# Kernel tuning notes

Hardware: AMD Instinct MI355X
Metric: run time of the kernel (lower is better)

Reference implementation:

```python
import jax, jax.numpy as jnp
import numpy as np

NMS_THRESH = 0.3  # default nms_thresh in DetNet.predict


def setup_inputs() -> dict:
    key = jax.random.key(0)
    k1, k2, k3, k4 = jax.random.split(key, 4)
    W, N = 8, 1024
    det = jax.random.uniform(k1, (W, N, 5), dtype=jnp.float32)          # (conf, cx, cy, w, h) in [0,1)
    offsets = jax.random.uniform(k2, (W, 5), dtype=jnp.float32) * 0.5   # window offset vector (0, left, top, 0, 0)-like
    scales = jax.random.uniform(k3, (W, 5), dtype=jnp.float32) * 0.5 + 0.25  # window scale vector
    b = jax.random.uniform(k4, (W, 4), dtype=jnp.float32)
    # (valid_left, valid_right, valid_top, valid_bottom) with left<right, top<bottom
    bounds = jnp.stack([0.3 * b[:, 0], 0.7 + 0.3 * b[:, 1],
                        0.3 * b[:, 2], 0.7 + 0.3 * b[:, 3]], axis=-1)
    return {"det": det, "offsets": offsets, "scales": scales, "bounds": bounds}


def _pairwise_iou(boxes):
    # boxes: [M,4] in (x1,y1,x2,y2)
    x1, y1, x2, y2 = boxes[:, 0], boxes[:, 1], boxes[:, 2], boxes[:, 3]
    area = jnp.clip(x2 - x1, 0.0) * jnp.clip(y2 - y1, 0.0)              # [M]
    iw = jnp.clip(jnp.minimum(x2[:, None], x2[None, :]) - jnp.maximum(x1[:, None], x1[None, :]), 0.0)
    ih = jnp.clip(jnp.minimum(y2[:, None], y2[None, :]) - jnp.maximum(y1[:, None], y1[None, :]), 0.0)
    inter = iw * ih                                                     # [M,M]
    union = area[:, None] + area[None, :] - inter
    return inter / jnp.maximum(union, 1e-9)


def reference(det, offsets, scales, bounds):
    W, N, _ = det.shape
    M = W * N
    cx, cy = det[..., 1], det[..., 2]                                    # [W,N]
    left, right = bounds[:, 0:1], bounds[:, 1:2]
    top, bottom = bounds[:, 2:3], bounds[:, 3:4]
    valid = (cx < right) & (cx > left) & (cy < bottom) & (cy > top)      # [W,N] border mask
    # torch.addcmul(offset, d, scale) = offset + d * scale
    d = (offsets[:, None, :] + det * scales[:, None, :]).reshape(M, 5)
    valid = valid.reshape(M)
    scores = jnp.where(valid, d[:, 0], -1.0)                             # invalid boxes never kept
    order = jnp.argsort(-scores)                                         # descending confidence
    d_s = d[order]                                                       # [M,5]
    s_s = scores[order]
    # point_form: (cx,cy,w,h) -> (x1,y1,x2,y2)
    cxy, wh = d_s[:, 1:3], d_s[:, 3:5]
    boxes = jnp.concatenate([cxy - wh * 0.5, cxy + wh * 0.5], axis=-1)
    iou = jax.lax.stop_gradient(_pairwise_iou(boxes))                    # [M,M], suppression is non-diff
    s_c = jax.lax.stop_gradient(s_s)
    idx = jnp.arange(M)

    def body(i, keep):
        # suppressed if any kept higher-score box overlaps > thresh
        sup = jnp.any(keep & (idx < i) & (iou[:, i] > NMS_THRESH))
        return keep.at[i].set(jnp.logical_and(~sup, s_c[i] > 0.0))

    keep = jax.lax.fori_loop(0, M, body, jnp.ones((M,), dtype=bool))
    return d_s * keep[:, None].astype(d_s.dtype)                         # [M,5], suppressed rows zeroed
```

## Files before the change

kernel.cpp:

```cpp
#include <hip/hip_runtime.h>
#include <cstdint>


#define M_TOT 8192
#define NMS_T 0.3f

#define WS_BOX   65536
#define WS_D     196608
#define WS_VCNT  360448
#define WS_ZROW  393216
#define WS_MASK  524288

typedef unsigned long long u64t;

__device__ __forceinline__ uint32_t desc_key(float sv) {
    uint32_t u = __float_as_uint(sv);
    uint32_t m = (u & 0x80000000u) ? ~u : (u | 0x80000000u);
    return ~m;
}

__device__ __forceinline__ u64t rdl64(u64t v, int sl) {
    unsigned lo = (unsigned)__builtin_amdgcn_readlane((int)(unsigned)v, sl);
    unsigned hi = (unsigned)__builtin_amdgcn_readlane((int)(unsigned)(v >> 32), sl);
    return ((u64t)hi << 32) | lo;
}

__device__ __forceinline__ int scatter_one(
    int i, int rank, u64t key,
    const float* __restrict__ det, const float* __restrict__ offsets,
    const float* __restrict__ scales,
    float4* __restrict__ boxes_srt, float* __restrict__ d_srt)
{
    uint32_t dkey = (uint32_t)(key >> 16);
    if (dkey >= 0x7FFFFFFFu) return 0;
    int g = i >> 10;
    float d0 = __fadd_rn(offsets[g*5+0], __fmul_rn(det[i*5+0], scales[g*5+0]));
    float d1 = __fadd_rn(offsets[g*5+1], __fmul_rn(det[i*5+1], scales[g*5+1]));
    float d2 = __fadd_rn(offsets[g*5+2], __fmul_rn(det[i*5+2], scales[g*5+2]));
    float d3 = __fadd_rn(offsets[g*5+3], __fmul_rn(det[i*5+3], scales[g*5+3]));
    float d4 = __fadd_rn(offsets[g*5+4], __fmul_rn(det[i*5+4], scales[g*5+4]));
    d_srt[rank*5+0] = d0; d_srt[rank*5+1] = d1; d_srt[rank*5+2] = d2;
    d_srt[rank*5+3] = d3; d_srt[rank*5+4] = d4;
    float hw = __fmul_rn(d3, 0.5f), hh = __fmul_rn(d4, 0.5f);
    boxes_srt[rank] = make_float4(__fsub_rn(d1, hw), __fsub_rn(d2, hh),
                                  __fadd_rn(d1, hw), __fadd_rn(d2, hh));
    return 1;
}

__global__ __launch_bounds__(256) void k2_rank(
    const float* __restrict__ det, const float* __restrict__ offsets,
    const float* __restrict__ scales, const float* __restrict__ bounds,
    float4* __restrict__ boxes_srt, float* __restrict__ d_srt,
    unsigned int* __restrict__ vcnt, u64t* __restrict__ zrow,
    float* __restrict__ out)
{
    __shared__ u64t skey[M_TOT];
    __shared__ float soff[40], sscl[40], sbnd[32];
    __shared__ int sTop;
    int t = threadIdx.x;
    int lane = t & 63;
    if (t == 0) sTop = 0;
    if (t < 40) { soff[t] = offsets[t]; sscl[t] = scales[t]; }
    if (t < 32) { sbnd[t] = bounds[t]; }
    if (blockIdx.x == 0 && t < 128) zrow[t] = 0ull;
    __syncthreads();

    #pragma unroll 4
    for (int s = 0; s < 32; ++s) {
        int u = s * 256 + t;
        int g = u >> 10;
        float raw_s = det[u * 5 + 0];
        float cx    = det[u * 5 + 1];
        float cy    = det[u * 5 + 2];
        float score = __fadd_rn(soff[g * 5 + 0], __fmul_rn(raw_s, sscl[g * 5 + 0]));
        bool valid = (cx < sbnd[g*4+1]) && (cx > sbnd[g*4+0]) &&
                     (cy < sbnd[g*4+3]) && (cy > sbnd[g*4+2]);
        float sv = valid ? score : -1.0f;
        uint32_t dk = desc_key(sv);
        bool push = dk < 0x7FFFFFFFu;
        u64t key = ((u64t)dk << 16) | (unsigned)u;
        u64t bal = __ballot(push);
        if (bal) {
            int lw = 0;
            if (lane == 0) lw = atomicAdd(&sTop, __popcll(bal));
            int wbase = __builtin_amdgcn_readfirstlane(lw);
            if (push) {
                int off = __popcll(bal & ((1ull << lane) - 1ull));
                skey[wbase + off] = key;
            }
        }
    }
    __syncthreads();
    int V = sTop;
    int Vpad = (V + 15) & ~15;
    if (t < Vpad - V) skey[V + t] = ~0ull;
    {
        int zb = blockIdx.x * 160;
        for (int z = zb + t; z < zb + 160; z += 256) out[z] = 0.0f;
    }
    __syncthreads();
    if (t == 0) *vcnt = (unsigned)V;

    int grp = t >> 3;
    int jq  = t & 7;
    int i = blockIdx.x * 32 + grp;
    int g = i >> 10;
    float raw_s = det[i * 5 + 0];
    float cx    = det[i * 5 + 1];
    float cy    = det[i * 5 + 2];
    float score = __fadd_rn(soff[g * 5 + 0], __fmul_rn(raw_s, sscl[g * 5 + 0]));
    bool valid = (cx < sbnd[g*4+1]) && (cx > sbnd[g*4+0]) &&
                 (cy < sbnd[g*4+3]) && (cy > sbnd[g*4+2]);
    float sv = valid ? score : -1.0f;
    uint32_t dk = desc_key(sv);
    u64t ki = ((u64t)dk << 16) | (unsigned)i;
    const ulonglong2* skey2 = (const ulonglong2*)skey;
    int c = 0;
    int nit = Vpad >> 4;
    #pragma unroll 4
    for (int it = 0; it < nit; ++it) {
        ulonglong2 kj = skey2[it * 8 + jq];
        c += (kj.x < ki) + (kj.y < ki);
    }
    c += __shfl_xor(c, 1);
    c += __shfl_xor(c, 2);
    c += __shfl_xor(c, 4);
    if (jq == 0)
        scatter_one(i, c, ki, det, offsets, scales, boxes_srt, d_srt);
}

__global__ __launch_bounds__(256) void k_mask(
    const float4* __restrict__ boxes_srt,
    const unsigned int* __restrict__ vcnt,
    u64t* __restrict__ mask)
{
    __shared__ float4 sb[16 * 65];
    __shared__ float  sa[16 * 65];
    int V = (int)*vcnt;
    int bx = blockIdx.x, by = blockIdx.y;
    if (bx * 32 >= V) return;
    if (by * 1024 >= V) return;
    if (by * 16 + 15 < (bx * 32) >> 6) return;
    int nc = (V + 63) >> 6;
    int tid = threadIdx.x;
    int cbase = by * 1024;
    for (int u = tid; u < 1024; u += 256) {
        float4 b = boxes_srt[cbase + u];
        int c = u >> 6, jj = u & 63;
        sb[c * 65 + jj] = b;
        sa[c * 65 + jj] = __fmul_rn(fmaxf(__fsub_rn(b.z, b.x), 0.0f),
                                    fmaxf(__fsub_rn(b.w, b.y), 0.0f));
    }
    __syncthreads();
    int r = bx * 32 + (tid >> 3);
    if (r >= V) return;
    float4 bi = boxes_srt[r];
    float ai = __fmul_rn(fmaxf(__fsub_rn(bi.z, bi.x), 0.0f),
                         fmaxf(__fsub_rn(bi.w, bi.y), 0.0f));
    int rw = r >> 6;
    #pragma unroll
    for (int k = 0; k < 2; ++k) {
        int wl = (tid & 7) + k * 8;
        int w = by * 16 + wl;
        if (w < rw || w >= nc) continue;
        u64t bits = 0;
        #pragma unroll 4
        for (int jj = 0; jj < 64; ++jj) {
            float4 bj = sb[wl * 65 + jj];
            float aj = sa[wl * 65 + jj];
            float iw = fmaxf(__fsub_rn(fminf(bi.z, bj.z), fmaxf(bi.x, bj.x)), 0.0f);
            float ih = fmaxf(__fsub_rn(fminf(bi.w, bj.w), fmaxf(bi.y, bj.y)), 0.0f);
            float inter = __fmul_rn(iw, ih);
            float uni   = __fsub_rn(__fadd_rn(ai, aj), inter);
            float iou   = __fdiv_rn(inter, fmaxf(uni, 1e-9f));
            int j = w * 64 + jj;
            if (j > r && iou > NMS_T) bits |= 1ull << jj;
        }
        mask[(size_t)r * 128 + w] = bits;
    }
}

struct WSlot { ulonglong2 dl, dh, n1l, n1h, n2l, n2h; };

__device__ __forceinline__ void fill_words(
    const u64t* __restrict__ mask, int lane, int T, WSlot& w)
{
    int rl = min(T * 128 + lane,      M_TOT - 1);
    int rh = min(T * 128 + 64 + lane, M_TOT - 1);
    const ulonglong2* mrl = (const ulonglong2*)(mask + (size_t)rl * 128);
    const ulonglong2* mrh = (const ulonglong2*)(mask + (size_t)rh * 128);
    int p0 = min(T,     63);
    int p1 = min(T + 1, 63);
    int p2 = min(T + 2, 63);
    w.dl  = mrl[p0]; w.dh  = mrh[p0];
    w.n1l = mrl[p1]; w.n1h = mrh[p1];
    w.n2l = mrl[p2]; w.n2h = mrh[p2];
}

__device__ __forceinline__ void res_step(
    const u64t* __restrict__ mask,
    u64t* sdead, u64t* ck, volatile int* res_prog, volatile int* h_prog,
    int lane, int nc, int T,
    u64t& cA_lo, u64t& cA_hi, u64t& cB_lo, u64t& cB_hi, WSlot& w)
{
    if (T >= 3) {
        int need = T - 2;
        while (true) {
            int hp = (lane < 7) ? h_prog[lane] : 0x7FFFFFFF;
            if (__ballot(hp < need) == 0ull) break;
        }
    }
    u64t dlo = ((volatile u64t*)sdead)[2 * T];
    u64t dhi = ((volatile u64t*)sdead)[2 * T + 1];
    u64t live_lo = ~(dlo | cA_lo);
    u64t live_hi = ~(dhi | cA_hi);
    u64t km_lo = 0, km_hi = 0, c1l = 0, c1h = 0, c2l = 0, c2h = 0;
    while (live_lo | live_hi) {
        if (live_lo) {
            int bs = __builtin_amdgcn_readfirstlane(__builtin_ctzll(live_lo));
            u64t rml = rdl64(w.dl.x, bs), rmh = rdl64(w.dl.y, bs);
            c1l |= rdl64(w.n1l.x, bs); c1h |= rdl64(w.n1l.y, bs);
            c2l |= rdl64(w.n2l.x, bs); c2h |= rdl64(w.n2l.y, bs);
            km_lo |= 1ull << bs;
            live_lo &= ~rml & ~(1ull << bs);
            live_hi &= ~rmh;
        } else {
            int bs = __builtin_amdgcn_readfirstlane(__builtin_ctzll(live_hi));
            u64t rmh = rdl64(w.dh.y, bs);
            c1l |= rdl64(w.n1h.x, bs); c1h |= rdl64(w.n1h.y, bs);
            c2l |= rdl64(w.n2h.x, bs); c2h |= rdl64(w.n2h.y, bs);
            km_hi |= 1ull << bs;
            live_hi &= ~rmh & ~(1ull << bs);
        }
    }
    if (lane == 0) { ck[2 * T] = km_lo; ck[2 * T + 1] = km_hi; }
    __threadfence_block();
    if (lane == 0) *res_prog = T + 1;
    cA_lo = cB_lo | c1l; cA_hi = cB_hi | c1h;
    cB_lo = c2l;         cB_hi = c2h;
    fill_words(mask, lane, T + 3, w);
}

__global__ __launch_bounds__(512) void k3_serial(
    const u64t* __restrict__ mask, const u64t* __restrict__ zrow,
    const float* __restrict__ d_srt, const unsigned int* __restrict__ vcnt,
    float* __restrict__ out)
{
    __shared__ u64t sdead[128];
    __shared__ u64t ck[128];
    __shared__ int  res_prog;
    __shared__ int  h_prog[7];
    int tid = threadIdx.x, wv = tid >> 6, lane = tid & 63;
    int V = (int)*vcnt;
    int nc = (V + 127) >> 7;
    if (tid < 128) {
        int bw = tid * 64;
        u64t w0 = 0;
        if (bw >= V)           w0 = ~0ull;
        else if (bw + 64 > V)  w0 = (~0ull) << (V - bw);
        sdead[tid] = w0;
        ck[tid] = 0ull;
    }
    if (tid == 0) res_prog = 0;
    if (tid < 7)  h_prog[tid] = tid;
    __syncthreads();

    if (wv == 0) {
        u64t cA_lo = 0, cA_hi = 0, cB_lo = 0, cB_hi = 0;
        WSlot WA, WB, WC;
        fill_words(mask, lane, 0, WA);
        fill_words(mask, lane, 1, WB);
        fill_words(mask, lane, 2, WC);
        for (int t = 0; t < nc; t += 3) {
            res_step(mask, sdead, ck, &res_prog, h_prog, lane, nc, t,
                     cA_lo, cA_hi, cB_lo, cB_hi, WA);
            if (t + 1 < nc)
                res_step(mask, sdead, ck, &res_prog, h_prog, lane, nc, t + 1,
                         cA_lo, cA_hi, cB_lo, cB_hi, WB);
            if (t + 2 < nc)
                res_step(mask, sdead, ck, &res_prog, h_prog, lane, nc, t + 2,
                         cA_lo, cA_hi, cB_lo, cB_hi, WC);
        }
    } else {
        int hh = wv - 1;
        for (int c = hh; c < nc; c += 7) {
            while (*(volatile int*)&res_prog <= c) __builtin_amdgcn_s_sleep(1);
            u64t kl = ((volatile u64t*)ck)[2 * c];
            u64t kh = ((volatile u64t*)ck)[2 * c + 1];
            if (kl | kh) {
                int base = c * 128;
                u64t ax = 0, ay = 0;
                while (kl | kh) {
                    ulonglong2 b[4];
                    #pragma unroll
                    for (int q = 0; q < 4; ++q) {
                        const ulonglong2* ptr;
                        if (kl) {
                            int b_ = __builtin_ctzll(kl); kl &= kl - 1;
                            ptr = (const ulonglong2*)(mask + (size_t)(base + b_) * 128) + lane;
                        } else if (kh) {
                            int b_ = __builtin_ctzll(kh); kh &= kh - 1;
                            ptr = (const ulonglong2*)(mask + (size_t)(base + 64 + b_) * 128) + lane;
                        } else {
                            ptr = (const ulonglong2*)zrow + lane;
                        }
                        b[q] = *ptr;
                    }
                    ax |= b[0].x | b[1].x | b[2].x | b[3].x;
                    ay |= b[0].y | b[1].y | b[2].y | b[3].y;
                }
                atomicOr(&sdead[2 * lane],     ax);
                atomicOr(&sdead[2 * lane + 1], ay);
            }
            __threadfence_block();
            if (lane == 0) ((volatile int*)h_prog)[hh] = c + 7;
        }
        if (lane == 0) ((volatile int*)h_prog)[hh] = 0x7FFFFFFF;
    }
    __syncthreads();
    if (tid < 128) {
        u64t m = ck[tid];
        while (m) {
            int b = __builtin_ctzll(m); m &= m - 1;
            int rr = tid * 64 + b;
            out[rr * 5 + 0] = d_srt[rr * 5 + 0];
            out[rr * 5 + 1] = d_srt[rr * 5 + 1];
            out[rr * 5 + 2] = d_srt[rr * 5 + 2];
            out[rr * 5 + 3] = d_srt[rr * 5 + 3];
            out[rr * 5 + 4] = d_srt[rr * 5 + 4];
        }
    }
}

extern "C" void kernel_launch(void* const* d_in, const int* in_sizes, int n_in,
                              void* d_out, int out_size, void* d_ws, size_t ws_size,
                              hipStream_t stream) {
    const float* det     = (const float*)d_in[0];
    const float* offsets = (const float*)d_in[1];
    const float* scales  = (const float*)d_in[2];
    const float* bounds  = (const float*)d_in[3];
    float* out = (float*)d_out;
    char* ws = (char*)d_ws;
    float4*       boxes = (float4*)(ws + WS_BOX);
    float*        d_srt = (float*)(ws + WS_D);
    unsigned int* vcnt  = (unsigned int*)(ws + WS_VCNT);
    u64t*         zrow  = (u64t*)(ws + WS_ZROW);
    u64t*         mask  = (u64t*)(ws + WS_MASK);

    k2_rank<<<256, 256, 0, stream>>>(det, offsets, scales, bounds, boxes, d_srt, vcnt, zrow, out);
    k_mask<<<dim3(256, 8), 256, 0, stream>>>(boxes, vcnt, mask);
    k3_serial<<<1, 512, 0, stream>>>(mask, zrow, d_srt, vcnt, out);
}
```

Measured before the change: 162.0 us.

## Shrink serial NMS chunks to 64 rows and stage diagonal mask band in LDS

The serial resolve wave now handles 64-row chunks instead of 128, and it preloads the diagonal and next two mask words for the first 64 chunks into shared memory before resolution starts. The scan only reads a lane word for each kept box, and the lookahead suppression words are gathered after the kept set is published, so helper waves can start sooner. The aim is to shorten the latency-bound serial critical path by removing global loads and the lo/hi branching from each step. In exchange it adds twice as many chunk handoffs between waves and a large LDS allocation that must be filled up front.

```diff
diff --git a/kernel.cpp b/kernel.cpp
--- a/kernel.cpp
+++ b/kernel.cpp
@@ -4,6 +4,7 @@
 
 #define M_TOT 8192
 #define NMS_T 0.3f
+#define PCMAX 64
 
 #define WS_BOX   65536
 #define WS_D     196608
@@ -18,21 +19,25 @@
     uint32_t m = (u & 0x80000000u) ? ~u : (u | 0x80000000u);
     return ~m;
 }
-
 __device__ __forceinline__ u64t rdl64(u64t v, int sl) {
     unsigned lo = (unsigned)__builtin_amdgcn_readlane((int)(unsigned)v, sl);
     unsigned hi = (unsigned)__builtin_amdgcn_readlane((int)(unsigned)(v >> 32), sl);
     return ((u64t)hi << 32) | lo;
 }
-
-__device__ __forceinline__ int scatter_one(
+__device__ __forceinline__ u64t rdfl64(u64t v) {
+    unsigned lo = (unsigned)__builtin_amdgcn_readfirstlane((int)(unsigned)v);
+    unsigned hi = (unsigned)__builtin_amdgcn_readfirstlane((int)(unsigned)(v >> 32));
+    return ((u64t)hi << 32) | lo;
+}
+
+__device__ __forceinline__ void scatter_one(
     int i, int rank, u64t key,
     const float* __restrict__ det, const float* __restrict__ offsets,
     const float* __restrict__ scales,
     float4* __restrict__ boxes_srt, float* __restrict__ d_srt)
 {
     uint32_t dkey = (uint32_t)(key >> 16);
-    if (dkey >= 0x7FFFFFFFu) return 0;
+    if (dkey >= 0x7FFFFFFFu) return;
     int g = i >> 10;
     float d0 = __fadd_rn(offsets[g*5+0], __fmul_rn(det[i*5+0], scales[g*5+0]));
     float d1 = __fadd_rn(offsets[g*5+1], __fmul_rn(det[i*5+1], scales[g*5+1]));
@@ -44,7 +49,6 @@
     float hw = __fmul_rn(d3, 0.5f), hh = __fmul_rn(d4, 0.5f);
     boxes_srt[rank] = make_float4(__fsub_rn(d1, hw), __fsub_rn(d2, hh),
                                   __fadd_rn(d1, hw), __fadd_rn(d2, hh));
-    return 1;
 }
 
 __global__ __launch_bounds__(256) void k2_rank(
@@ -180,79 +184,22 @@
     }
 }
 
-struct WSlot { ulonglong2 dl, dh, n1l, n1h, n2l, n2h; };
-
-__device__ __forceinline__ void fill_words(
-    const u64t* __restrict__ mask, int lane, int T, WSlot& w)
-{
-    int rl = min(T * 128 + lane,      M_TOT - 1);
-    int rh = min(T * 128 + 64 + lane, M_TOT - 1);
-    const ulonglong2* mrl = (const ulonglong2*)(mask + (size_t)rl * 128);
-    const ulonglong2* mrh = (const ulonglong2*)(mask + (size_t)rh * 128);
-    int p0 = min(T,     63);
-    int p1 = min(T + 1, 63);
-    int p2 = min(T + 2, 63);
-    w.dl  = mrl[p0]; w.dh  = mrh[p0];
-    w.n1l = mrl[p1]; w.n1h = mrh[p1];
-    w.n2l = mrl[p2]; w.n2h = mrh[p2];
-}
-
-__device__ __forceinline__ void res_step(
-    const u64t* __restrict__ mask,
-    u64t* sdead, u64t* ck, volatile int* res_prog, volatile int* h_prog,
-    int lane, int nc, int T,
-    u64t& cA_lo, u64t& cA_hi, u64t& cB_lo, u64t& cB_hi, WSlot& w)
-{
-    if (T >= 3) {
-        int need = T - 2;
-        while (true) {
-            int hp = (lane < 7) ? h_prog[lane] : 0x7FFFFFFF;
-            if (__ballot(hp < need) == 0ull) break;
-        }
-    }
-    u64t dlo = ((volatile u64t*)sdead)[2 * T];
-    u64t dhi = ((volatile u64t*)sdead)[2 * T + 1];
-    u64t live_lo = ~(dlo | cA_lo);
-    u64t live_hi = ~(dhi | cA_hi);
-    u64t km_lo = 0, km_hi = 0, c1l = 0, c1h = 0, c2l = 0, c2h = 0;
-    while (live_lo | live_hi) {
-        if (live_lo) {
-            int bs = __builtin_amdgcn_readfirstlane(__builtin_ctzll(live_lo));
-            u64t rml = rdl64(w.dl.x, bs), rmh = rdl64(w.dl.y, bs);
-            c1l |= rdl64(w.n1l.x, bs); c1h |= rdl64(w.n1l.y, bs);
-            c2l |= rdl64(w.n2l.x, bs); c2h |= rdl64(w.n2l.y, bs);
-            km_lo |= 1ull << bs;
-            live_lo &= ~rml & ~(1ull << bs);
-            live_hi &= ~rmh;
-        } else {
-            int bs = __builtin_amdgcn_readfirstlane(__builtin_ctzll(live_hi));
-            u64t rmh = rdl64(w.dh.y, bs);
-            c1l |= rdl64(w.n1h.x, bs); c1h |= rdl64(w.n1h.y, bs);
-            c2l |= rdl64(w.n2h.x, bs); c2h |= rdl64(w.n2h.y, bs);
-            km_hi |= 1ull << bs;
-            live_hi &= ~rmh & ~(1ull << bs);
-        }
-    }
-    if (lane == 0) { ck[2 * T] = km_lo; ck[2 * T + 1] = km_hi; }
-    __threadfence_block();
-    if (lane == 0) *res_prog = T + 1;
-    cA_lo = cB_lo | c1l; cA_hi = cB_hi | c1h;
-    cB_lo = c2l;         cB_hi = c2h;
-    fill_words(mask, lane, T + 3, w);
-}
 
 __global__ __launch_bounds__(512) void k3_serial(
     const u64t* __restrict__ mask, const u64t* __restrict__ zrow,
     const float* __restrict__ d_srt, const unsigned int* __restrict__ vcnt,
     float* __restrict__ out)
 {
+    __shared__ u64t sband[PCMAX * 64 * 3];
     __shared__ u64t sdead[128];
     __shared__ u64t ck[128];
     __shared__ int  res_prog;
     __shared__ int  h_prog[7];
     int tid = threadIdx.x, wv = tid >> 6, lane = tid & 63;
     int V = (int)*vcnt;
-    int nc = (V + 127) >> 7;
+    int nc = (V + 63) >> 6;
+    int PC = min(nc, PCMAX);
+
     if (tid < 128) {
         int bw = tid * 64;
         u64t w0 = 0;
@@ -263,34 +210,67 @@
     }
     if (tid == 0) res_prog = 0;
     if (tid < 7)  h_prog[tid] = tid;
+    for (int e = tid; e < PC * 64; e += 512) {
+        int c = e >> 6;
+        const u64t* rp = mask + (size_t)e * 128;
+        sband[e * 3 + 0] = rp[c];
+        sband[e * 3 + 1] = rp[c + 1];
+        sband[e * 3 + 2] = rp[c + 2];
+    }
     __syncthreads();
 
     if (wv == 0) {
-        u64t cA_lo = 0, cA_hi = 0, cB_lo = 0, cB_hi = 0;
-        WSlot WA, WB, WC;
-        fill_words(mask, lane, 0, WA);
-        fill_words(mask, lane, 1, WB);
-        fill_words(mask, lane, 2, WC);
-        for (int t = 0; t < nc; t += 3) {
-            res_step(mask, sdead, ck, &res_prog, h_prog, lane, nc, t,
-                     cA_lo, cA_hi, cB_lo, cB_hi, WA);
-            if (t + 1 < nc)
-                res_step(mask, sdead, ck, &res_prog, h_prog, lane, nc, t + 1,
-                         cA_lo, cA_hi, cB_lo, cB_hi, WB);
-            if (t + 2 < nc)
-                res_step(mask, sdead, ck, &res_prog, h_prog, lane, nc, t + 2,
-                         cA_lo, cA_hi, cB_lo, cB_hi, WC);
+        u64t cA = 0, cB = 0;
+        for (int T = 0; T < nc; ++T) {
+            u64t d, n1, n2;
+            if (T < PC) {
+                const u64t* p = sband + (size_t)(T * 64 + lane) * 3;
+                d = p[0]; n1 = p[1]; n2 = p[2];
+            } else {
+                int r = min(T * 64 + lane, M_TOT - 1);
+                const u64t* rp = mask + (size_t)r * 128;
+                int w = min(T, 125);
+                d = rp[w]; n1 = rp[w + 1]; n2 = rp[w + 2];
+            }
+            if (T >= 3) {
+                int need = T - 2;
+                while (true) {
+                    int hp = (lane < 7) ? h_prog[lane] : 0x7FFFFFFF;
+                    if (__ballot(hp < need) == 0ull) break;
+                }
+            }
+            u64t dead = rdfl64(((volatile u64t*)sdead)[T]) | cA;
+            u64t live = ~dead;
+            int rem = V - T * 64;
+            if (rem < 64) live &= (1ull << rem) - 1ull;
+            u64t km = 0;
+            while (live) {
+                int bs = (int)__builtin_ctzll(live);
+                km |= 1ull << bs;
+                u64t rm = rdl64(d, bs);
+                live &= ~rm & ~(1ull << bs);
+            }
+            if (lane == 0) ck[T] = km;
+            __threadfence_block();
+            if (lane == 0) *(volatile int*)&res_prog = T + 1;
+            u64t c1 = 0, c2 = 0, k2m = km;
+            while (k2m) {
+                int b = (int)__builtin_ctzll(k2m); k2m &= k2m - 1;
+                c1 |= rdl64(n1, b);
+                c2 |= rdl64(n2, b);
+            }
+            cA = cB | c1;
+            cB = c2;
         }
     } else {
         int hh = wv - 1;
         for (int c = hh; c < nc; c += 7) {
             while (*(volatile int*)&res_prog <= c) __builtin_amdgcn_s_sleep(1);
-            u64t kl = ((volatile u64t*)ck)[2 * c];
-            u64t kh = ((volatile u64t*)ck)[2 * c + 1];
-            if (kl | kh) {
-                int base = c * 128;
+            u64t kl = ((volatile u64t*)ck)[c];
+            if (kl) {
+                int base = c * 64;
                 u64t ax = 0, ay = 0;
-                while (kl | kh) {
+                while (kl) {
                     ulonglong2 b[4];
                     #pragma unroll
                     for (int q = 0; q < 4; ++q) {
@@ -298,9 +278,6 @@
                         if (kl) {
                             int b_ = __builtin_ctzll(kl); kl &= kl - 1;
                             ptr = (const ulonglong2*)(mask + (size_t)(base + b_) * 128) + lane;
-                        } else if (kh) {
-                            int b_ = __builtin_ctzll(kh); kh &= kh - 1;
-                            ptr = (const ulonglong2*)(mask + (size_t)(base + 64 + b_) * 128) + lane;
                         } else {
                             ptr = (const ulonglong2*)zrow + lane;
                         }
```

After: 148.2 us. 8.5% less time.
